# Kernel tuning notes

Measured on AMD Instinct MI355X. Metric: run time of the kernel, lower is better.

Reference implementation:

```python
import jax, jax.numpy as jnp
import numpy as np
import math

D = 768
H = 12
DFF = 3072
HD = D // H


def _layernorm(x, g, b, eps=1e-5):
    mu = jnp.mean(x, axis=-1, keepdims=True)
    var = jnp.var(x, axis=-1, keepdims=True)
    return (x - mu) * jax.lax.rsqrt(var + eps) * g + b


def setup_inputs() -> dict:
    key = jax.random.key(0)
    ks = jax.random.split(key, 12)
    B, S = 2, 4096
    s = 1.0 / math.sqrt(D)
    sf = 1.0 / math.sqrt(DFF)
    return {
        "x": jax.random.normal(ks[0], (B, S, D), jnp.float32),
        "attention_mask": jnp.ones((B, S), jnp.int32),
        "ln1_g": jnp.ones((D,), jnp.float32),
        "ln1_b": jnp.zeros((D,), jnp.float32),
        "ln2_g": jnp.ones((D,), jnp.float32),
        "ln2_b": jnp.zeros((D,), jnp.float32),
        "Wq": jax.random.normal(ks[1], (D, D), jnp.float32) * s,
        "bq": jnp.zeros((D,), jnp.float32),
        "Wk": jax.random.normal(ks[2], (D, D), jnp.float32) * s,
        "bk": jnp.zeros((D,), jnp.float32),
        "Wv": jax.random.normal(ks[3], (D, D), jnp.float32) * s,
        "bv": jnp.zeros((D,), jnp.float32),
        "Wo": jax.random.normal(ks[4], (D, D), jnp.float32) * s,
        "bo": jnp.zeros((D,), jnp.float32),
        "W1": jax.random.normal(ks[5], (D, DFF), jnp.float32) * s,
        "b1": jnp.zeros((DFF,), jnp.float32),
        "W2": jax.random.normal(ks[6], (DFF, D), jnp.float32) * sf,
        "b2": jnp.zeros((D,), jnp.float32),
    }


def _block(x, attention_mask, ln1_g, ln1_b, ln2_g, ln2_b,
           Wq, bq, Wk, bk, Wv, bv, Wo, bo, W1, b1, W2, b2):
    B, S, _ = x.shape
    h = _layernorm(x, ln1_g, ln1_b)
    q = (h @ Wq + bq).reshape(B, S, H, HD)
    k = (h @ Wk + bk).reshape(B, S, H, HD)
    v = (h @ Wv + bv).reshape(B, S, H, HD)
    # scores: [B, H, S, S]
    dots = jnp.einsum('bqhd,bkhd->bhqk', q, k) / math.sqrt(HD)
    causal = jnp.tril(jnp.ones((S, S), bool))  # True = keep
    keep = causal[None, None] & (attention_mask != 0)[:, None, None, :]
    dots = jnp.where(keep, dots, -jnp.inf)
    probs = jax.nn.softmax(dots, axis=-1)
    ctx = jnp.einsum('bhqk,bkhd->bqhd', probs, v).reshape(B, S, D)
    sa = ctx @ Wo + bo  # dropout = identity (eval)
    x = x + sa
    h2 = _layernorm(x, ln2_g, ln2_b)
    ff = jax.nn.relu(h2 @ W1 + b1) @ W2 + b2
    return x + ff


def reference(x, attention_mask, ln1_g, ln1_b, ln2_g, ln2_b,
              Wq, bq, Wk, bk, Wv, bv, Wo, bo, W1, b1, W2, b2):
    return _block(x, attention_mask, ln1_g, ln1_b, ln2_g, ln2_b,
                  Wq, bq, Wk, bk, Wv, bv, Wo, bo, W1, b1, W2, b2)
```

## Files before the change

kernel.cpp:

```cpp
#include <hip/hip_runtime.h>
#include <hip/hip_bf16.h>
#include <math.h>

#define S_LEN 4096
#define DMODEL 768
#define NHEAD 12
#define HDIM 64
#define DFF_ 3072
#define MROWS 8192

typedef __bf16 bf16;
typedef __bf16 bf16x4 __attribute__((ext_vector_type(4)));
typedef __bf16 bf16x8 __attribute__((ext_vector_type(8)));
typedef float f32x4 __attribute__((ext_vector_type(4)));

union F4 { float4 v; float f[4]; };
union U2 { bf16 h[2]; unsigned u; };
union U8 { unsigned u[4]; bf16x8 v; };

__device__ __forceinline__ void gld_lds16(void* lds, const void* g) {
    __builtin_amdgcn_global_load_lds(
        (const __attribute__((address_space(1))) unsigned int*)g,
        (__attribute__((address_space(3))) unsigned int*)lds, 16, 0, 0);
}

template<typename OUT>
__global__ __launch_bounds__(256) void ln_kernel(const float* __restrict__ x,
                                                 const float* __restrict__ g,
                                                 const float* __restrict__ bta,
                                                 OUT* __restrict__ out) {
    const int row = blockIdx.x;
    const int t = threadIdx.x;
    const float* xr = x + (size_t)row * DMODEL;
    float v0 = xr[t], v1 = xr[t + 256], v2 = xr[t + 512];
    float s = v0 + v1 + v2;
    float ss = v0 * v0 + v1 * v1 + v2 * v2;
    for (int o = 32; o > 0; o >>= 1) {
        s += __shfl_down(s, o, 64);
        ss += __shfl_down(ss, o, 64);
    }
    __shared__ float sm[4], sm2[4];
    const int w = t >> 6, lane = t & 63;
    if (lane == 0) { sm[w] = s; sm2[w] = ss; }
    __syncthreads();
    s = sm[0] + sm[1] + sm[2] + sm[3];
    ss = sm2[0] + sm2[1] + sm2[2] + sm2[3];
    const float mu = s * (1.0f / DMODEL);
    const float var = ss * (1.0f / DMODEL) - mu * mu;
    const float rs = rsqrtf(var + 1e-5f);
    OUT* orow = out + (size_t)row * DMODEL;
    orow[t]       = (OUT)((v0 - mu) * rs * g[t]       + bta[t]);
    orow[t + 256] = (OUT)((v1 - mu) * rs * g[t + 256] + bta[t + 256]);
    orow[t + 512] = (OUT)((v2 - mu) * rs * g[t + 512] + bta[t + 512]);
}

__global__ __launch_bounds__(256) void wtrans_all_kernel(
    const float* __restrict__ Wq, const float* __restrict__ Wk,
    const float* __restrict__ Wv, const float* __restrict__ Wo,
    const float* __restrict__ W1, const float* __restrict__ W2,
    bf16* __restrict__ Wqt, bf16* __restrict__ Wkt, bf16* __restrict__ Wvt,
    bf16* __restrict__ Wot, bf16* __restrict__ W1t, bf16* __restrict__ W2t) {
    int t = blockIdx.x;
    const float* W; bf16* Wt; int K, N;
    if      (t < 144)  { W = Wq; Wt = Wqt; K = 768;  N = 768;  }
    else if (t < 288)  { W = Wk; Wt = Wkt; K = 768;  N = 768;  t -= 144; }
    else if (t < 432)  { W = Wv; Wt = Wvt; K = 768;  N = 768;  t -= 288; }
    else if (t < 576)  { W = Wo; Wt = Wot; K = 768;  N = 768;  t -= 432; }
    else if (t < 1152) { W = W1; Wt = W1t; K = 768;  N = 3072; t -= 576; }
    else               { W = W2; Wt = W2t; K = 3072; N = 768;  t -= 1152; }
    const int nx = N >> 6;
    const int n0 = (t % nx) * 64, k0 = (t / nx) * 64;

    __shared__ float tile[64][65];
    const int tid = threadIdx.x;
    const int lr = tid >> 4, lc = (tid & 15) << 2;
#pragma unroll
    for (int i = 0; i < 4; ++i) {
        const int r = lr + i * 16;
        F4 w; w.v = *(const float4*)&W[(size_t)(k0 + r) * N + n0 + lc];
#pragma unroll
        for (int j = 0; j < 4; ++j) tile[r][lc + j] = w.f[j];
    }
    __syncthreads();
#pragma unroll
    for (int i = 0; i < 4; ++i) {
        const int n = lr + i * 16;
        bf16x4 o;
#pragma unroll
        for (int j = 0; j < 4; ++j) o[j] = (bf16)tile[lc + j][n];
        *(bf16x4*)&Wt[(size_t)(n0 + n) * K + k0 + lc] = o;
    }
}

template<int MT, bool RELU, bool RES, bool OUT_BF16>
__global__ __launch_bounds__(256) void mgemm_kernel(
    const bf16* __restrict__ A,
    const bf16* __restrict__ Wt0, const float* __restrict__ bias0, void* __restrict__ C0,
    const bf16* __restrict__ Wt1, const float* __restrict__ bias1, void* __restrict__ C1,
    const bf16* __restrict__ Wt2, const float* __restrict__ bias2, void* __restrict__ C2,
    const float* __restrict__ R, int M, int N, int K, int Kloop,
    int koff0, int koff1, int koff2,
    float sc0, float sc1, float sc2) {
    const bf16* Wt = Wt0; const float* bias = bias0; void* C = C0; float sc = sc0; int koff = koff0;
    if (blockIdx.z == 1) { Wt = Wt1; bias = bias1; C = C1; sc = sc1; koff = koff1; }
    if (blockIdx.z == 2) { Wt = Wt2; bias = bias2; C = C2; sc = sc2; koff = koff2; }

    constexpr int NI = (MT == 128) ? 4 : 2;
    __shared__ bf16 As[MT * 32];
    __shared__ bf16 Bs[128 * 32];

    const int tid = threadIdx.x;
    const int wave = tid >> 6, lane = tid & 63;
    const int row0 = blockIdx.y * MT, col0 = blockIdx.x * 128;
    const int wr = (MT == 128) ? (wave >> 1) * 64 : 0;
    const int wc = (MT == 128) ? (wave & 1) * 64 : wave * 32;
    const int mrow = lane & 15, kq = (lane >> 4) * 8;

    const int st_row = (lane >> 2);
    const int st_off = (lane & 3) * 16;

    f32x4 acc[4][NI] = {};

    const char* Ab = (const char*)(A + (size_t)row0 * K + koff);
    const char* Bb = (const char*)(Wt + (size_t)col0 * K + koff);
    const size_t strideA = (size_t)K * 2;

    for (int k0 = 0; k0 < Kloop; k0 += 32) {
        if (MT == 128) {
#pragma unroll
            for (int issue = 0; issue < 2; ++issue) {
                const int r = wave * 32 + issue * 16 + st_row;
                gld_lds16((char*)As + (wave * 32 + issue * 16) * 64,
                          Ab + (size_t)r * strideA + k0 * 2 + st_off);
            }
        } else {
            const int r = wave * 16 + st_row;
            gld_lds16((char*)As + (wave * 16) * 64,
                      Ab + (size_t)r * strideA + k0 * 2 + st_off);
        }
#pragma unroll
        for (int issue = 0; issue < 2; ++issue) {
            const int r = wave * 32 + issue * 16 + st_row;
            gld_lds16((char*)Bs + (wave * 32 + issue * 16) * 64,
                      Bb + (size_t)r * strideA + k0 * 2 + st_off);
        }
        __syncthreads();
        bf16x8 af[4], bfr[NI];
#pragma unroll
        for (int mi = 0; mi < 4; ++mi)
            af[mi] = *(const bf16x8*)&As[(wr + mi * 16 + mrow) * 32 + kq];
#pragma unroll
        for (int ni = 0; ni < NI; ++ni)
            bfr[ni] = *(const bf16x8*)&Bs[(wc + ni * 16 + mrow) * 32 + kq];
#pragma unroll
        for (int mi = 0; mi < 4; ++mi)
#pragma unroll
            for (int ni = 0; ni < NI; ++ni)
                acc[mi][ni] = __builtin_amdgcn_mfma_f32_16x16x32_bf16(
                    af[mi], bfr[ni], acc[mi][ni], 0, 0, 0);
        __syncthreads();
    }

    const int quad = lane >> 4;
    float bv[NI];
#pragma unroll
    for (int ni = 0; ni < NI; ++ni) bv[ni] = bias[col0 + wc + ni * 16 + mrow];
#pragma unroll
    for (int mi = 0; mi < 4; ++mi) {
#pragma unroll
        for (int r = 0; r < 4; ++r) {
            const int row = row0 + wr + mi * 16 + quad * 4 + r;
#pragma unroll
            for (int ni = 0; ni < NI; ++ni) {
                const int col = col0 + wc + ni * 16 + mrow;
                float v = acc[mi][ni][r] + bv[ni];
                if (RES) v += R[(size_t)row * N + col];
                v *= sc;
                if (RELU) v = fmaxf(v, 0.0f);
                if (OUT_BF16) ((bf16*)C)[(size_t)row * N + col] = (bf16)v;
                else          ((float*)C)[(size_t)row * N + col] = v;
            }
        }
    }
}

__global__ __launch_bounds__(256) void ff2_combine_kernel(
    const bf16* __restrict__ p0, const bf16* __restrict__ p1,
    const float* __restrict__ b2, const float* __restrict__ x1,
    float* __restrict__ out) {
    const int i = (blockIdx.x * 256 + threadIdx.x) * 4;
    bf16x4 a = *(const bf16x4*)(p0 + i);
    bf16x4 b = *(const bf16x4*)(p1 + i);
    F4 xr; xr.v = *(const float4*)(x1 + i);
    const int col = i % DMODEL;
    F4 o;
#pragma unroll
    for (int j = 0; j < 4; ++j)
        o.f[j] = (float)a[j] + (float)b[j] + b2[col + j] + xr.f[j];
    *(float4*)(out + i) = o.v;
}

__global__ __launch_bounds__(256) void mattn_kernel(
    const bf16* __restrict__ Q, const bf16* __restrict__ K,
    const bf16* __restrict__ V, const int* __restrict__ amask,
    bf16* __restrict__ O) {
    const int bx = blockIdx.x, h = blockIdx.y, b = blockIdx.z;

    __shared__ bf16 Ks[2][64][68];
    __shared__ bf16 Vt[2][64][68];
    __shared__ bf16 Os[64][68];
    __shared__ float mk[2][64];
    __shared__ int flagv[2];

    const int tid = threadIdx.x;
    const int wave = tid >> 6, lane = tid & 63;
    const int l = lane & 15, quad = lane >> 4;
    const int qh = quad >> 1;
    const int srcA = (quad & 1) * 32 + l;
    const int srcB = srcA + 16;
    const float NEG_INF = -__builtin_huge_valf();

    const int kr = tid >> 2, ks = (tid & 3) * 16;
    const int vk0 = (tid & 31) * 2, vds = (tid >> 5) * 8;

    const bf16* Kbase = K + (size_t)b * S_LEN * DMODEL + h * HDIM;
    const bf16* Vbase = V + (size_t)b * S_LEN * DMODEL + h * HDIM;

#pragma unroll 1
    for (int pass = 0; pass < 2; ++pass) {
        const int qt = pass ? bx : (63 - bx);

        const bf16* Qb = Q + (size_t)(b * S_LEN + qt * 64 + wave * 16 + l) * DMODEL + h * HDIM;
        const bf16x8 qf0 = *(const bf16x8*)(Qb + quad * 8);
        const bf16x8 qf1 = *(const bf16x8*)(Qb + 32 + quad * 8);

        float m_run = NEG_INF, l_run = 0.0f;
        f32x4 acc[4] = {};

        bf16x8 kp0, kp1, vp0, vp1;
        int mv = 1;
        {
            const bf16* kg = Kbase + (size_t)kr * DMODEL + ks;
            kp0 = *(const bf16x8*)kg;
            kp1 = *(const bf16x8*)(kg + 8);
            const bf16* vg = Vbase + (size_t)vk0 * DMODEL + vds;
            vp0 = *(const bf16x8*)vg;
            vp1 = *(const bf16x8*)(vg + DMODEL);
            if (wave == 0) mv = amask[b * S_LEN + lane];
        }
        __syncthreads();
        {
            *(bf16x8*)&Ks[0][kr][ks]     = kp0;
            *(bf16x8*)&Ks[0][kr][ks + 8] = kp1;
#pragma unroll
            for (int i = 0; i < 8; ++i) {
                U2 w; w.h[0] = vp0[i]; w.h[1] = vp1[i];
                *(unsigned*)&Vt[0][vds + i][vk0] = w.u;
            }
            if (wave == 0) {
                mk[0][lane] = mv ? 0.0f : NEG_INF;
                unsigned long long bal = __ballot(mv != 0);
                if (lane == 0) flagv[0] = (bal == ~0ULL);
            }
        }
        __syncthreads();
        int buf = 0;

        for (int kt = 0; kt <= qt; ++kt) {
            const bool more = (kt < qt);
            if (more) {
                const bf16* kg = Kbase + (size_t)((kt + 1) * 64 + kr) * DMODEL + ks;
                kp0 = *(const bf16x8*)kg;
                kp1 = *(const bf16x8*)(kg + 8);
                const bf16* vg = Vbase + (size_t)((kt + 1) * 64 + vk0) * DMODEL + vds;
                vp0 = *(const bf16x8*)vg;
                vp1 = *(const bf16x8*)(vg + DMODEL);
                if (wave == 0) mv = amask[b * S_LEN + (kt + 1) * 64 + lane];
            }

            const int allv = flagv[buf];
            f32x4 sreg[4] = {};
#pragma unroll
            for (int mi = 0; mi < 4; ++mi) {
                bf16x8 kf0 = *(const bf16x8*)&Ks[buf][mi * 16 + l][quad * 8];
                bf16x8 kf1 = *(const bf16x8*)&Ks[buf][mi * 16 + l][32 + quad * 8];
                sreg[mi] = __builtin_amdgcn_mfma_f32_16x16x32_bf16(kf0, qf0, sreg[mi], 0, 0, 0);
                sreg[mi] = __builtin_amdgcn_mfma_f32_16x16x32_bf16(kf1, qf1, sreg[mi], 0, 0, 0);
            }
            if (!allv) {
#pragma unroll
                for (int mi = 0; mi < 4; ++mi) {
                    F4 m4; m4.v = *(const float4*)&mk[buf][mi * 16 + quad * 4];
#pragma unroll
                    for (int r = 0; r < 4; ++r) sreg[mi][r] += m4.f[r];
                }
            }
            if (kt == qt) {
#pragma unroll
                for (int mi = 0; mi < 4; ++mi)
#pragma unroll
                    for (int r = 0; r < 4; ++r)
                        if (mi * 16 + quad * 4 + r > wave * 16 + l)
                            sreg[mi][r] = NEG_INF;
            }

            float mloc = sreg[0][0];
#pragma unroll
            for (int mi = 0; mi < 4; ++mi)
#pragma unroll
                for (int r = 0; r < 4; ++r) mloc = fmaxf(mloc, sreg[mi][r]);
            mloc = fmaxf(mloc, __shfl_xor(mloc, 16, 64));
            mloc = fmaxf(mloc, __shfl_xor(mloc, 32, 64));
            const float mn = fmaxf(m_run, mloc);
            const float alpha = __builtin_amdgcn_exp2f(m_run - mn);
            m_run = mn;
            float ls = 0.0f;
#pragma unroll
            for (int mi = 0; mi < 4; ++mi)
#pragma unroll
                for (int r = 0; r < 4; ++r) {
                    const float p = __builtin_amdgcn_exp2f(sreg[mi][r] - mn);
                    sreg[mi][r] = p;
                    ls += p;
                }
            ls += __shfl_xor(ls, 16, 64);
            ls += __shfl_xor(ls, 32, 64);
            l_run = l_run * alpha + ls;
#pragma unroll
            for (int mi = 0; mi < 4; ++mi)
#pragma unroll
                for (int r = 0; r < 4; ++r) acc[mi][r] *= alpha;

            unsigned pk[4][2];
#pragma unroll
            for (int mi = 0; mi < 4; ++mi) {
                U2 w0; w0.h[0] = (bf16)sreg[mi][0]; w0.h[1] = (bf16)sreg[mi][1];
                U2 w1; w1.h[0] = (bf16)sreg[mi][2]; w1.h[1] = (bf16)sreg[mi][3];
                pk[mi][0] = w0.u; pk[mi][1] = w1.u;
            }
            bf16x8 pfrag[2];
#pragma unroll
            for (int kc = 0; kc < 2; ++kc) {
                U8 u;
#pragma unroll
                for (int t = 0; t < 2; ++t) {
                    const unsigned a0 = (unsigned)__shfl((int)pk[2 * kc][t],     srcA, 64);
                    const unsigned b0 = (unsigned)__shfl((int)pk[2 * kc + 1][t], srcA, 64);
                    u.u[t] = qh ? b0 : a0;
                    const unsigned a1 = (unsigned)__shfl((int)pk[2 * kc][t],     srcB, 64);
                    const unsigned b1 = (unsigned)__shfl((int)pk[2 * kc + 1][t], srcB, 64);
                    u.u[2 + t] = qh ? b1 : a1;
                }
                pfrag[kc] = u.v;
            }
#pragma unroll
            for (int mi = 0; mi < 4; ++mi) {
                bf16x8 vf0 = *(const bf16x8*)&Vt[buf][mi * 16 + l][quad * 8];
                bf16x8 vf1 = *(const bf16x8*)&Vt[buf][mi * 16 + l][32 + quad * 8];
                acc[mi] = __builtin_amdgcn_mfma_f32_16x16x32_bf16(vf0, pfrag[0], acc[mi], 0, 0, 0);
                acc[mi] = __builtin_amdgcn_mfma_f32_16x16x32_bf16(vf1, pfrag[1], acc[mi], 0, 0, 0);
            }

            if (more) {
                const int nb = buf ^ 1;
                *(bf16x8*)&Ks[nb][kr][ks]     = kp0;
                *(bf16x8*)&Ks[nb][kr][ks + 8] = kp1;
#pragma unroll
                for (int i = 0; i < 8; ++i) {
                    U2 w; w.h[0] = vp0[i]; w.h[1] = vp1[i];
                    *(unsigned*)&Vt[nb][vds + i][vk0] = w.u;
                }
                if (wave == 0) {
                    mk[nb][lane] = mv ? 0.0f : NEG_INF;
                    unsigned long long bal = __ballot(mv != 0);
                    if (lane == 0) flagv[nb] = (bal == ~0ULL);
                }
            }
            __syncthreads();
            buf ^= 1;
        }

        const float rinv = 1.0f / l_run;
#pragma unroll
        for (int mi = 0; mi < 4; ++mi) {
            U2 w0; w0.h[0] = (bf16)(acc[mi][0] * rinv); w0.h[1] = (bf16)(acc[mi][1] * rinv);
            U2 w1; w1.h[0] = (bf16)(acc[mi][2] * rinv); w1.h[1] = (bf16)(acc[mi][3] * rinv);
            *(unsigned*)&Os[wave * 16 + l][mi * 16 + quad * 4]     = w0.u;
            *(unsigned*)&Os[wave * 16 + l][mi * 16 + quad * 4 + 2] = w1.u;
        }
        __syncthreads();
        {
            const int orow = tid >> 2, oseg = (tid & 3) * 16;
            bf16* Og = O + (size_t)(b * S_LEN + qt * 64 + orow) * DMODEL + h * HDIM + oseg;
            *(bf16x8*)Og       = *(const bf16x8*)&Os[orow][oseg];
            *(bf16x8*)(Og + 8) = *(const bf16x8*)&Os[orow][oseg + 8];
        }
    }
}

extern "C" void kernel_launch(void* const* d_in, const int* in_sizes, int n_in,
                              void* d_out, int out_size, void* d_ws, size_t ws_size,
                              hipStream_t stream) {
    const float* x     = (const float*)d_in[0];
    const int*   amask = (const int*)  d_in[1];
    const float* ln1_g = (const float*)d_in[2];
    const float* ln1_b = (const float*)d_in[3];
    const float* ln2_g = (const float*)d_in[4];
    const float* ln2_b = (const float*)d_in[5];
    const float* Wq = (const float*)d_in[6];  const float* bq = (const float*)d_in[7];
    const float* Wk = (const float*)d_in[8];  const float* bk = (const float*)d_in[9];
    const float* Wv = (const float*)d_in[10]; const float* bv = (const float*)d_in[11];
    const float* Wo = (const float*)d_in[12]; const float* bo = (const float*)d_in[13];
    const float* W1 = (const float*)d_in[14]; const float* b1 = (const float*)d_in[15];
    const float* W2 = (const float*)d_in[16]; const float* b2 = (const float*)d_in[17];
    float* out = (float*)d_out;

    char* ws = (char*)d_ws;
    const size_t WSML = (size_t)DMODEL * DMODEL * 2;
    const size_t WBIG = (size_t)DMODEL * DFF_ * 2;
    bf16* Wqt = (bf16*)(ws + 0 * WSML);
    bf16* Wkt = (bf16*)(ws + 1 * WSML);
    bf16* Wvt = (bf16*)(ws + 2 * WSML);
    bf16* Wot = (bf16*)(ws + 3 * WSML);
    bf16* W1t = (bf16*)(ws + 4 * WSML);
    bf16* W2t = (bf16*)(ws + 4 * WSML + WBIG);
    char* act = ws + 4 * WSML + 2 * WBIG;

    const size_t HB = (size_t)MROWS * DMODEL * 2;
    const size_t FB = (size_t)MROWS * DMODEL * 4;
    bf16*  h    = (bf16*)(act);
    bf16*  qb   = (bf16*)(act + HB);
    bf16*  kb   = (bf16*)(act + 2 * HB);
    bf16*  vb   = (bf16*)(act + 3 * HB);
    bf16*  ctx  = h;
    float* x1   = (float*)(act + 4 * HB);
    bf16*  f    = (bf16*)(act + 4 * HB + FB);
    bf16*  h2   = h;
    bf16*  p0   = qb;
    bf16*  p1   = kb;
    float* zbias = (float*)vb;

    const float SCL = 0.125f * 1.44269504089f;

    wtrans_all_kernel<<<1728, 256, 0, stream>>>(Wq, Wk, Wv, Wo, W1, W2,
                                                Wqt, Wkt, Wvt, Wot, W1t, W2t);

    ln_kernel<bf16><<<MROWS, 256, 0, stream>>>(x, ln1_g, ln1_b, h);
    mgemm_kernel<128, false, false, true><<<dim3(DMODEL / 128, MROWS / 128, 3), 256, 0, stream>>>(
        h, Wqt, bq, qb, Wkt, bk, kb, Wvt, bv, vb, nullptr,
        MROWS, DMODEL, DMODEL, DMODEL, 0, 0, 0, SCL, 1.0f, 1.0f);
    mattn_kernel<<<dim3(32, NHEAD, 2), 256, 0, stream>>>(qb, kb, vb, amask, ctx);
    hipMemsetAsync(zbias, 0, DMODEL * sizeof(float), stream);
    mgemm_kernel<64, false, true, false><<<dim3(DMODEL / 128, MROWS / 64, 1), 256, 0, stream>>>(
        ctx, Wot, bo, x1, Wot, bo, x1, Wot, bo, x1, x,
        MROWS, DMODEL, DMODEL, DMODEL, 0, 0, 0, 1.0f, 1.0f, 1.0f);
    ln_kernel<bf16><<<MROWS, 256, 0, stream>>>(x1, ln2_g, ln2_b, h2);
    mgemm_kernel<128, true, false, true><<<dim3(DFF_ / 128, MROWS / 128, 1), 256, 0, stream>>>(
        h2, W1t, b1, f, W1t, b1, f, W1t, b1, f, nullptr,
        MROWS, DFF_, DMODEL, DMODEL, 0, 0, 0, 1.0f, 1.0f, 1.0f);
    mgemm_kernel<128, false, false, true><<<dim3(DMODEL / 128, MROWS / 128, 2), 256, 0, stream>>>(
        f, W2t, zbias, p0, W2t, zbias, p1, W2t, zbias, p1, nullptr,
        MROWS, DMODEL, DFF_, DFF_ / 2, 0, DFF_ / 2, 0, 1.0f, 1.0f, 1.0f);
    ff2_combine_kernel<<<(MROWS * DMODEL) / 1024, 256, 0, stream>>>(p0, p1, b2, x1, out);
}
```

Before: 493.8 us.

## Use 16x16x16 MFMA for PV to drop shuffles; process two K-steps per GEMM sync

In the attention kernel, the P·V product now uses the 16x16x16 bf16 MFMA when the compiler provides it. That lets the packed probability registers feed the MFMA directly instead of being rearranged with cross-lane shuffles, at the cost of twice as many MFMA instructions and smaller LDS reads of V. In the GEMM kernel, each iteration now loads two 32-wide K slices into separate LDS buffers and computes both before syncing. This halves the number of barriers per K, but doubles LDS usage and assumes Kloop is a multiple of 64.

```diff
diff --git a/kernel.cpp b/kernel.cpp
--- a/kernel.cpp
+++ b/kernel.cpp
@@ -13,10 +13,27 @@
 typedef __bf16 bf16x4 __attribute__((ext_vector_type(4)));
 typedef __bf16 bf16x8 __attribute__((ext_vector_type(8)));
 typedef float f32x4 __attribute__((ext_vector_type(4)));
+typedef short s16x4 __attribute__((ext_vector_type(4)));
 
 union F4 { float4 v; float f[4]; };
 union U2 { bf16 h[2]; unsigned u; };
 union U8 { unsigned u[4]; bf16x8 v; };
+
+#if __has_builtin(__builtin_amdgcn_mfma_f32_16x16x16bf16_1k)
+typedef s16x4 mf16_t;
+#define MFMA16(a, b, c) __builtin_amdgcn_mfma_f32_16x16x16bf16_1k((a), (b), (c), 0, 0, 0)
+#define HAVE_MFMA16 1
+#elif __has_builtin(__builtin_amdgcn_mfma_f32_16x16x16_bf16)
+typedef bf16x4 mf16_t;
+#define MFMA16(a, b, c) __builtin_amdgcn_mfma_f32_16x16x16_bf16((a), (b), (c), 0, 0, 0)
+#define HAVE_MFMA16 1
+#else
+#define HAVE_MFMA16 0
+#endif
+
+#if HAVE_MFMA16
+union U4 { unsigned u[2]; mf16_t v; };
+#endif
 
 __device__ __forceinline__ void gld_lds16(void* lds, const void* g) {
     __builtin_amdgcn_global_load_lds(
@@ -106,8 +123,8 @@
     if (blockIdx.z == 2) { Wt = Wt2; bias = bias2; C = C2; sc = sc2; koff = koff2; }
 
     constexpr int NI = (MT == 128) ? 4 : 2;
-    __shared__ bf16 As[MT * 32];
-    __shared__ bf16 Bs[128 * 32];
+    __shared__ bf16 As[2][MT * 32];
+    __shared__ bf16 Bs[2][128 * 32];
 
     const int tid = threadIdx.x;
     const int wave = tid >> 6, lane = tid & 63;
@@ -125,39 +142,46 @@
     const char* Bb = (const char*)(Wt + (size_t)col0 * K + koff);
     const size_t strideA = (size_t)K * 2;
 
-    for (int k0 = 0; k0 < Kloop; k0 += 32) {
-        if (MT == 128) {
+    for (int k0 = 0; k0 < Kloop; k0 += 64) {
+#pragma unroll
+        for (int s = 0; s < 2; ++s) {
+            const int kk = k0 + s * 32;
+            if (MT == 128) {
+#pragma unroll
+                for (int issue = 0; issue < 2; ++issue) {
+                    const int r = wave * 32 + issue * 16 + st_row;
+                    gld_lds16((char*)As[s] + (wave * 32 + issue * 16) * 64,
+                              Ab + (size_t)r * strideA + kk * 2 + st_off);
+                }
+            } else {
+                const int r = wave * 16 + st_row;
+                gld_lds16((char*)As[s] + (wave * 16) * 64,
+                          Ab + (size_t)r * strideA + kk * 2 + st_off);
+            }
 #pragma unroll
             for (int issue = 0; issue < 2; ++issue) {
                 const int r = wave * 32 + issue * 16 + st_row;
-                gld_lds16((char*)As + (wave * 32 + issue * 16) * 64,
-                          Ab + (size_t)r * strideA + k0 * 2 + st_off);
-            }
-        } else {
-            const int r = wave * 16 + st_row;
-            gld_lds16((char*)As + (wave * 16) * 64,
-                      Ab + (size_t)r * strideA + k0 * 2 + st_off);
-        }
-#pragma unroll
-        for (int issue = 0; issue < 2; ++issue) {
-            const int r = wave * 32 + issue * 16 + st_row;
-            gld_lds16((char*)Bs + (wave * 32 + issue * 16) * 64,
-                      Bb + (size_t)r * strideA + k0 * 2 + st_off);
+                gld_lds16((char*)Bs[s] + (wave * 32 + issue * 16) * 64,
+                          Bb + (size_t)r * strideA + kk * 2 + st_off);
+            }
         }
         __syncthreads();
-        bf16x8 af[4], bfr[NI];
-#pragma unroll
-        for (int mi = 0; mi < 4; ++mi)
-            af[mi] = *(const bf16x8*)&As[(wr + mi * 16 + mrow) * 32 + kq];
-#pragma unroll
-        for (int ni = 0; ni < NI; ++ni)
-            bfr[ni] = *(const bf16x8*)&Bs[(wc + ni * 16 + mrow) * 32 + kq];
-#pragma unroll
-        for (int mi = 0; mi < 4; ++mi)
+#pragma unroll
+        for (int s = 0; s < 2; ++s) {
+            bf16x8 af[4], bfr[NI];
+#pragma unroll
+            for (int mi = 0; mi < 4; ++mi)
+                af[mi] = *(const bf16x8*)&As[s][(wr + mi * 16 + mrow) * 32 + kq];
 #pragma unroll
             for (int ni = 0; ni < NI; ++ni)
-                acc[mi][ni] = __builtin_amdgcn_mfma_f32_16x16x32_bf16(
-                    af[mi], bfr[ni], acc[mi][ni], 0, 0, 0);
+                bfr[ni] = *(const bf16x8*)&Bs[s][(wc + ni * 16 + mrow) * 32 + kq];
+#pragma unroll
+            for (int mi = 0; mi < 4; ++mi)
+#pragma unroll
+                for (int ni = 0; ni < NI; ++ni)
+                    acc[mi][ni] = __builtin_amdgcn_mfma_f32_16x16x32_bf16(
+                        af[mi], bfr[ni], acc[mi][ni], 0, 0, 0);
+        }
         __syncthreads();
     }
 
@@ -215,9 +239,11 @@
     const int tid = threadIdx.x;
     const int wave = tid >> 6, lane = tid & 63;
     const int l = lane & 15, quad = lane >> 4;
+#if !HAVE_MFMA16
     const int qh = quad >> 1;
     const int srcA = (quad & 1) * 32 + l;
     const int srcB = srcA + 16;
+#endif
     const float NEG_INF = -__builtin_huge_valf();
 
     const int kr = tid >> 2, ks = (tid & 3) * 16;
@@ -338,6 +364,18 @@
                 U2 w1; w1.h[0] = (bf16)sreg[mi][2]; w1.h[1] = (bf16)sreg[mi][3];
                 pk[mi][0] = w0.u; pk[mi][1] = w1.u;
             }
+
+#if HAVE_MFMA16
+#pragma unroll
+            for (int mi = 0; mi < 4; ++mi) {
+                U4 pb; pb.u[0] = pk[mi][0]; pb.u[1] = pk[mi][1];
+#pragma unroll
+                for (int di = 0; di < 4; ++di) {
+                    mf16_t va = *(const mf16_t*)&Vt[buf][di * 16 + l][mi * 16 + quad * 4];
+                    acc[di] = MFMA16(va, pb.v, acc[di]);
+                }
+            }
+#else
             bf16x8 pfrag[2];
 #pragma unroll
             for (int kc = 0; kc < 2; ++kc) {
@@ -360,6 +398,7 @@
                 acc[mi] = __builtin_amdgcn_mfma_f32_16x16x32_bf16(vf0, pfrag[0], acc[mi], 0, 0, 0);
                 acc[mi] = __builtin_amdgcn_mfma_f32_16x16x32_bf16(vf1, pfrag[1], acc[mi], 0, 0, 0);
             }
+#endif
 
             if (more) {
                 const int nb = buf ^ 1;
```

Measured after the change: 469.9 us. 1.05x faster.
